# Kernel optimization log

Measured on AMD Instinct MI355X. Metric: run time of the kernel, lower is better.

The kernel has to match this reference:

```python
import jax, jax.numpy as jnp
import numpy as np
from jax.scipy.special import logsumexp

B, T, D, H, K = 64, 800, 80, 128, 39  # batch, frames, feat dim, LSTM hidden/dir, num phones


def setup_inputs() -> dict:
    key = jax.random.key(0)
    ks = jax.random.split(key, 16)
    s = 0.1
    inp = {
        "features": jax.random.normal(ks[0], (B, T, D), jnp.float32),
        "lengths": jax.random.randint(ks[1], (B,), T // 2, T + 1, dtype=jnp.int32),
        "labels": jax.random.randint(ks[2], (B, T), 0, K, dtype=jnp.int32),
        # BiLSTM params (PyTorch layout: W_ih (4H,D), W_hh (4H,H); gate order i,f,g,o)
        "Wih_f": jax.random.normal(ks[3], (4 * H, D), jnp.float32) * s,
        "Whh_f": jax.random.normal(ks[4], (4 * H, H), jnp.float32) * s,
        "bih_f": jax.random.normal(ks[5], (4 * H,), jnp.float32) * s,
        "bhh_f": jax.random.normal(ks[6], (4 * H,), jnp.float32) * s,
        "Wih_b": jax.random.normal(ks[7], (4 * H, D), jnp.float32) * s,
        "Whh_b": jax.random.normal(ks[8], (4 * H, H), jnp.float32) * s,
        "bih_b": jax.random.normal(ks[9], (4 * H,), jnp.float32) * s,
        "bhh_b": jax.random.normal(ks[10], (4 * H,), jnp.float32) * s,
        # emission projection Linear(2H -> K)
        "Wp": jax.random.normal(ks[11], (K, 2 * H), jnp.float32) * s,
        "bp": jax.random.normal(ks[12], (K,), jnp.float32) * s,
        # CRF params (pytorch-crf init: U(-0.1, 0.1))
        "start_t": jax.random.uniform(ks[13], (K,), jnp.float32, -0.1, 0.1),
        "end_t": jax.random.uniform(ks[14], (K,), jnp.float32, -0.1, 0.1),
        "trans": jax.random.uniform(ks[15], (K, K), jnp.float32, -0.1, 0.1),
    }
    return inp


def _lstm(x, Wih, Whh, bih, bhh, reverse):
    """Single-direction LSTM over padded batch. x: (B,T,D) -> (B,T,H)."""
    nB, nT, _ = x.shape
    nH = Whh.shape[1]
    xW = jnp.swapaxes(x @ Wih.T + (bih + bhh), 0, 1)  # (T,B,4H)

    def step(carry, g):
        h, c = carry
        g = g + h @ Whh.T
        i, f, gg, o = jnp.split(g, 4, axis=-1)
        c = jax.nn.sigmoid(f) * c + jax.nn.sigmoid(i) * jnp.tanh(gg)
        h = jax.nn.sigmoid(o) * jnp.tanh(c)
        return (h, c), h

    init = (jnp.zeros((nB, nH), x.dtype), jnp.zeros((nB, nH), x.dtype))
    _, hs = jax.lax.scan(step, init, xW, reverse=reverse)
    return jnp.swapaxes(hs, 0, 1)  # (B,T,H)


def _crf_nll(emissions, labels, lengths, start_t, end_t, trans):
    """pytorch-crf: -mean log-likelihood. emissions (B,T,K), labels (B,T)."""
    nB, nT, nK = emissions.shape
    mask = (jnp.arange(nT)[None, :] < lengths[:, None])  # (B,T)
    mf = mask.astype(emissions.dtype)
    bidx = jnp.arange(nB)

    # --- numerator: score of gold path ---
    num = start_t[labels[:, 0]] + emissions[bidx, 0, labels[:, 0]]
    tr = trans[labels[:, :-1], labels[:, 1:]]  # (B,T-1)
    em = jnp.take_along_axis(emissions[:, 1:], labels[:, 1:, None], axis=2)[..., 0]
    num = num + ((tr + em) * mf[:, 1:]).sum(axis=1)
    last_tags = jnp.take_along_axis(labels, (lengths - 1)[:, None], axis=1)[:, 0]
    num = num + end_t[last_tags]

    # --- denominator: forward algorithm ---
    alpha0 = start_t[None, :] + emissions[:, 0]  # (B,K)
    em_rest = jnp.swapaxes(emissions[:, 1:], 0, 1)  # (T-1,B,K)
    m_rest = jnp.swapaxes(mask[:, 1:], 0, 1)  # (T-1,B)

    def step(alpha, inputs):
        em_t, m_t = inputs
        nxt = logsumexp(alpha[:, :, None] + trans[None] + em_t[:, None, :], axis=1)
        return jnp.where(m_t[:, None], nxt, alpha), None

    alpha, _ = jax.lax.scan(step, alpha0, (em_rest, m_rest))
    denom = logsumexp(alpha + end_t[None, :], axis=1)

    return -(num - denom).mean()


def reference(features, lengths, labels, Wih_f, Whh_f, bih_f, bhh_f,
              Wih_b, Whh_b, bih_b, bhh_b, Wp, bp, start_t, end_t, trans):
    h_f = _lstm(features, Wih_f, Whh_f, bih_f, bhh_f, reverse=False)
    h_b = _lstm(features, Wih_b, Whh_b, bih_b, bhh_b, reverse=True)
    hidden = jnp.concatenate([h_f, h_b], axis=-1)  # (B,T,2H)
    emissions = hidden @ Wp.T + bp  # (B,T,K)
    return _crf_nll(emissions, labels, lengths, start_t, end_t, trans)
```

## Files before the change

### kernel.cpp

```cpp
#include <hip/hip_runtime.h>
#include <cstddef>
#include <cstdint>

#define B_ 64
#define T_ 800
#define D_ 80
#define H_ 128
#define K_ 39
#define BT_ (B_ * T_)

#define NL2E_  (-1.44269504f)
#define N2L2E_ (-2.88539008f)

typedef _Float16 h2_t  __attribute__((ext_vector_type(2)));
typedef _Float16 f16x8 __attribute__((ext_vector_type(8)));
typedef float    f32x4 __attribute__((ext_vector_type(4)));
typedef uint32_t u32x4 __attribute__((ext_vector_type(4)));

__device__ __forceinline__ float fdot2_(h2_t a, h2_t b, float c) {
#if __has_builtin(__builtin_amdgcn_fdot2)
  return __builtin_amdgcn_fdot2(a, b, c, false);
#else
  return c + (float)a.x * (float)b.x + (float)a.y * (float)b.y;
#endif
}

__device__ __forceinline__ h2_t asH2u_(uint32_t u) { return __builtin_bit_cast(h2_t, u); }

__device__ __forceinline__ float ex2_(float x) {
#if __has_builtin(__builtin_amdgcn_exp2f)
  return __builtin_amdgcn_exp2f(x);
#else
  return __builtin_exp2f(x);
#endif
}
__device__ __forceinline__ float rcpf_(float x) {
#if __has_builtin(__builtin_amdgcn_rcpf)
  return __builtin_amdgcn_rcpf(x);
#else
  return 1.0f / x;
#endif
}
__device__ __forceinline__ float tanhf_(float x) { return 2.0f / (1.0f + __expf(-2.0f * x)) - 1.0f; }

__device__ __forceinline__ float laneb_(float v, int lane) {
  return __builtin_bit_cast(float, __builtin_amdgcn_readlane(__builtin_bit_cast(int, v), lane));
}
__device__ __forceinline__ uint32_t lanebu_(uint32_t v, int lane) {
  return (uint32_t)__builtin_amdgcn_readlane((int)v, lane);
}

__device__ __forceinline__ float dppswap1_(float v) {
  return __builtin_bit_cast(float,
    __builtin_amdgcn_mov_dpp(__builtin_bit_cast(int, v), 0xB1, 0xF, 0xF, true));
}

__device__ __forceinline__ void barrier_lds_() {
  asm volatile("s_waitcnt lgkmcnt(0)" ::: "memory");
  __builtin_amdgcn_s_barrier();
}

__device__ __forceinline__ void rows_of_(int tid, int& unit, int& role, int& r0, int& r1) {
  const int w = tid >> 6, L = tid & 63;
  unit = w * 32 + (L >> 1);
  role = L & 1;
  r0 = role * H_ + unit;
  r1 = 2 * H_ + role * H_ + unit;
}

template<int USE_XW>
__global__ __launch_bounds__(256, 1)
void lstm_kernel(const float* __restrict__ x,
                 const float* __restrict__ Wih_f, const float* __restrict__ Whh_f,
                 const float* __restrict__ bih_f, const float* __restrict__ bhh_f,
                 const float* __restrict__ Wih_b, const float* __restrict__ Whh_b,
                 const float* __restrict__ bih_b, const float* __restrict__ bhh_b,
                 _Float16* __restrict__ xw,
                 _Float16* __restrict__ hcat)
{
  const int bb  = blockIdx.x & 63;
  const int dir = blockIdx.x >> 6;
  const float* Whh = dir ? Whh_b : Whh_f;
  const float* Wih = dir ? Wih_b : Wih_f;
  const float* bih = dir ? bih_b : bih_f;
  const float* bhh = dir ? bhh_b : bhh_f;

  const int tid  = threadIdx.x;
  const int lane = tid & 63;

  __shared__ alignas(16) _Float16 hsf[2][H_];
  __shared__ uint32_t xs2[2][64];
  __shared__ alignas(16) _Float16 xs[128 * 96];

  if (USE_XW) {
    const int w    = tid >> 6;
    const int lm   = lane & 15;
    const int quad = lane >> 4;
    const int selw = w >> 1;
    const int rolw = w & 1;

    f16x8 Bf[8][3];
    #pragma unroll
    for (int nt = 0; nt < 8; ++nt) {
      const int r = w * 128 + nt * 16 + lm;
      const float fac = (r >= 256 && r < 384) ? N2L2E_ : NL2E_;
      #pragma unroll
      for (int kt = 0; kt < 3; ++kt) {
        const int kb = kt * 32 + quad * 8;
        #pragma unroll
        for (int j = 0; j < 8; ++j) {
          const int k = kb + j;
          Bf[nt][kt][j] = (k < D_) ? (_Float16)(fac * Wih[(size_t)r * D_ + k]) : (_Float16)0.0f;
        }
      }
    }

    for (int i = tid; i < 128 * 96; i += 256) xs[i] = (_Float16)0.0f;

    for (int cc = 0; cc < 7; ++cc) {
      const int base = cc * 128;
      const int nrow = (T_ - base < 128) ? (T_ - base) : 128;
      __syncthreads();
      {
        const float4* src = (const float4*)(x + ((size_t)bb * T_ + base) * D_);
        for (int i = tid; i < nrow * 20; i += 256) {
          float4 v = src[i];
          const int row = i / 20, col = (i % 20) * 4;
          h2_t p0, p1;
          p0.x = (_Float16)v.x; p0.y = (_Float16)v.y;
          p1.x = (_Float16)v.z; p1.y = (_Float16)v.w;
          uint2 pk;
          pk.x = __builtin_bit_cast(uint32_t, p0);
          pk.y = __builtin_bit_cast(uint32_t, p1);
          *(uint2*)&xs[row * 96 + col] = pk;
        }
      }
      __syncthreads();

      #pragma unroll
      for (int mt = 0; mt < 8; ++mt) {
        if (base + mt * 16 >= T_) break;
        f16x8 Af[3];
        #pragma unroll
        for (int kt = 0; kt < 3; ++kt)
          Af[kt] = *(const f16x8*)&xs[(mt * 16 + lm) * 96 + kt * 32 + quad * 8];

        f32x4 acc[8];
        #pragma unroll
        for (int nt = 0; nt < 8; ++nt) acc[nt] = (f32x4){0.f, 0.f, 0.f, 0.f};
        #pragma unroll
        for (int kt = 0; kt < 3; ++kt)
          #pragma unroll
          for (int nt = 0; nt < 8; ++nt)
            acc[nt] = __builtin_amdgcn_mfma_f32_16x16x32_f16(Af[kt], Bf[nt][kt], acc[nt], 0, 0, 0);

        #pragma unroll
        for (int nt = 0; nt < 8; ++nt) {
          const int unit = nt * 16 + lm;
          const int ptid = (unit >> 5) * 64 + (unit & 31) * 2 + rolw;
          #pragma unroll
          for (int rg = 0; rg < 4; ++rg) {
            const int t = base + mt * 16 + quad * 4 + rg;
            if (t < T_)
              xw[((size_t)dir * BT_ + (size_t)bb * T_ + t) * 512 + ptid * 2 + selw]
                = (_Float16)acc[nt][rg];
          }
        }
      }
    }
    __syncthreads();
  }

  const int Q = lane & 3; (void)Q;
  int unit, role, r0, r1; rows_of_(tid, unit, role, r0, r1);
  const float s0 = NL2E_;
  const float s1 = role ? NL2E_ : N2L2E_;
  const float qk2 = role ? 0.0f : -1.0f;

  h2_t w0[64], w1[64];
  #pragma unroll
  for (int j = 0; j < 64; ++j) {
    float2 a = *(const float2*)(Whh + (size_t)r0 * H_ + 2 * j);
    float2 d = *(const float2*)(Whh + (size_t)r1 * H_ + 2 * j);
    w0[j].x = (_Float16)(s0 * a.x); w0[j].y = (_Float16)(s0 * a.y);
    w1[j].x = (_Float16)(s1 * d.x); w1[j].y = (_Float16)(s1 * d.y);
  }
  h2_t wx0[40], wx1[40];
  if (!USE_XW) {
    #pragma unroll
    for (int i = 0; i < 40; ++i) {
      float2 a = *(const float2*)(Wih + (size_t)r0 * D_ + 2 * i);
      float2 d = *(const float2*)(Wih + (size_t)r1 * D_ + 2 * i);
      wx0[i].x = (_Float16)(s0 * a.x); wx0[i].y = (_Float16)(s0 * a.y);
      wx1[i].x = (_Float16)(s1 * d.x); wx1[i].y = (_Float16)(s1 * d.y);
    }
  }
  const float bias0 = s0 * (bih[r0] + bhh[r0]);
  const float bias1 = s1 * (bih[r1] + bhh[r1]);

  if (tid < H_) hsf[0][tid] = (_Float16)0.0f;
  if (!USE_XW && tid < 64) { xs2[0][tid] = 0u; xs2[1][tid] = 0u; }
  float c = 0.0f;

  const uint32_t* xwdu = (const uint32_t*)xw + ((size_t)dir * BT_ + (size_t)bb * T_) * 256;
  const float*    xb   = x + (size_t)bb * T_ * D_;
  _Float16*       hb   = hcat + (size_t)bb * T_ * (2 * H_) + dir * H_;

  _Float16* hbp = hb + (size_t)(dir ? (T_ - 1) : 0) * (2 * H_);
  const ptrdiff_t hstep = dir ? -(2 * H_) : (2 * H_);
  int xoff = (dir ? (T_ - 3) : 2) * 256 + tid;
  const int xstep = dir ? -256 : 256;

  uint32_t xwA = 0u, xwB = 0u;
  h2_t xpend; xpend.x = (_Float16)0.f; xpend.y = (_Float16)0.f;
  {
    const int tq0 = dir ? (T_ - 1) : 0;
    const int tq1 = dir ? (T_ - 2) : 1;
    if (USE_XW) {
      xwA = xwdu[(size_t)tq0 * 256 + tid];
      xwB = xwdu[(size_t)tq1 * 256 + tid];
    } else if (tid < 40) {
      float2 v0 = *(const float2*)(xb + (size_t)tq0 * D_ + 2 * tid);
      h2_t p; p.x = (_Float16)v0.x; p.y = (_Float16)v0.y;
      xs2[0][tid] = __builtin_bit_cast(uint32_t, p);
      float2 v1 = *(const float2*)(xb + (size_t)tq1 * D_ + 2 * tid);
      xpend.x = (_Float16)v1.x; xpend.y = (_Float16)v1.y;
    }
  }
  __syncthreads();

  auto step = [&](int tt, int par, uint32_t& xwreg) {
    float a0, a1, a2, a3, b0, b1, b2, b3;
    if (USE_XW) {
      const h2_t xv = asH2u_(xwreg);
      a0 = bias0 + (float)xv.x;
      b0 = bias1 + (float)xv.y;
      a1 = a2 = a3 = 0.f; b1 = b2 = b3 = 0.f;
      xwreg = xwdu[xoff];
    } else {
      a0 = bias0; b0 = bias1;
      a1 = a2 = a3 = 0.f; b1 = b2 = b3 = 0.f;
      if (tid < 40) {
        xs2[par ^ 1][tid] = __builtin_bit_cast(uint32_t, xpend);
        const int ttc = (tt + 2 < T_) ? (tt + 2) : (T_ - 1);
        const int tq2 = dir ? (T_ - 1 - ttc) : ttc;
        float2 v = *(const float2*)(xb + (size_t)tq2 * D_ + 2 * tid);
        xpend.x = (_Float16)v.x; xpend.y = (_Float16)v.y;
      }
      uint32_t xreg = xs2[par][lane];
      #pragma unroll
      for (int j = 0; j < 40; j += 4) {
        h2_t q0 = asH2u_(lanebu_(xreg, j));
        h2_t q1 = asH2u_(lanebu_(xreg, j + 1));
        h2_t q2 = asH2u_(lanebu_(xreg, j + 2));
        h2_t q3 = asH2u_(lanebu_(xreg, j + 3));
        a0 = fdot2_(wx0[j],     q0, a0); b0 = fdot2_(wx1[j],     q0, b0);
        a1 = fdot2_(wx0[j + 1], q1, a1); b1 = fdot2_(wx1[j + 1], q1, b1);
        a2 = fdot2_(wx0[j + 2], q2, a2); b2 = fdot2_(wx1[j + 2], q2, b2);
        a3 = fdot2_(wx0[j + 3], q3, a3); b3 = fdot2_(wx1[j + 3], q3, b3);
      }
    }

    const u32x4* hq = (const u32x4*)hsf[par];
    #pragma unroll
    for (int g = 0; g < 16; ++g) {
      const u32x4 hv = hq[g];
      a0 = fdot2_(w0[4 * g + 0], asH2u_(hv[0]), a0);
      b0 = fdot2_(w1[4 * g + 0], asH2u_(hv[0]), b0);
      a1 = fdot2_(w0[4 * g + 1], asH2u_(hv[1]), a1);
      b1 = fdot2_(w1[4 * g + 1], asH2u_(hv[1]), b1);
      a2 = fdot2_(w0[4 * g + 2], asH2u_(hv[2]), a2);
      b2 = fdot2_(w1[4 * g + 2], asH2u_(hv[2]), b2);
      a3 = fdot2_(w0[4 * g + 3], asH2u_(hv[3]), a3);
      b3 = fdot2_(w1[4 * g + 3], asH2u_(hv[3]), b3);
    }
    const float ga = (a0 + a1) + (a2 + a3);
    const float gb = (b0 + b1) + (b2 + b3);

    const float ea = ex2_(ga);
    const float sg = rcpf_(1.0f + ea);
    const float gbc = fminf(fmaxf(gb, -34.6f), 34.6f);
    const float eb = ex2_(gbc);
    const float qv = fmaf(qk2, eb, 1.0f) * rcpf_(1.0f + eb);
    const float ex = dppswap1_(sg * qv);
    c = fmaf(sg, c, ex);
    const float hn = qv * tanhf_(c);
    if (role) {
      hsf[par ^ 1][unit] = (_Float16)hn;
      hbp[unit] = (_Float16)hn;
    }
    hbp += hstep;
    if (tt + 3 < T_) xoff += xstep;
    barrier_lds_();
  };

  for (int tb = 0; tb < T_; tb += 2) {
    step(tb,     0, xwA);
    step(tb + 1, 1, xwB);
  }
}

__global__ __launch_bounds__(256, 1)
void emis_kernel(const _Float16* __restrict__ hcat,
                 const float* __restrict__ Wp, const float* __restrict__ bp,
                 float* __restrict__ em)
{
  const int tid  = threadIdx.x;
  const int w    = tid >> 6;
  const int lane = tid & 63;
  const int lm   = lane & 15;
  const int quad = lane >> 4;

  f16x8 Bf[3][8];
  float bias[3];
  #pragma unroll
  for (int nt = 0; nt < 3; ++nt) {
    const int n = nt * 16 + lm;
    const bool valid = n < K_;
    bias[nt] = valid ? bp[n] : 0.0f;
    #pragma unroll
    for (int kt = 0; kt < 8; ++kt) {
      const int kb = kt * 32 + quad * 8;
      #pragma unroll
      for (int j = 0; j < 8; ++j)
        Bf[nt][kt][j] = valid ? (_Float16)Wp[(size_t)n * 256 + kb + j] : (_Float16)0.0f;
    }
  }

  #pragma unroll
  for (int q = 0; q < 4; ++q) {
    const int mt  = blockIdx.x * 16 + w * 4 + q;
    const int bt0 = mt * 16;

    f16x8 Af[8];
    const _Float16* ab = hcat + ((size_t)bt0 + lm) * 256;
    #pragma unroll
    for (int kt = 0; kt < 8; ++kt)
      Af[kt] = *(const f16x8*)(ab + kt * 32 + quad * 8);

    f32x4 acc[3];
    #pragma unroll
    for (int nt = 0; nt < 3; ++nt) acc[nt] = (f32x4){0.f, 0.f, 0.f, 0.f};
    #pragma unroll
    for (int kt = 0; kt < 8; ++kt)
      #pragma unroll
      for (int nt = 0; nt < 3; ++nt)
        acc[nt] = __builtin_amdgcn_mfma_f32_16x16x32_f16(Af[kt], Bf[nt][kt], acc[nt], 0, 0, 0);

    #pragma unroll
    for (int nt = 0; nt < 3; ++nt) {
      const int n = nt * 16 + lm;
      if (n < K_) {
        #pragma unroll
        for (int rg = 0; rg < 4; ++rg) {
          const int row = bt0 + quad * 4 + rg;
          em[(size_t)row * K_ + n] = acc[nt][rg] + bias[nt];
        }
      }
    }
  }
}

__global__ __launch_bounds__(256)
void crf_dn_kernel(const float* __restrict__ em,
                   const int* __restrict__ labels, const int* __restrict__ lengths,
                   const float* __restrict__ start_t, const float* __restrict__ end_t,
                   const float* __restrict__ trans,
                   float* __restrict__ dn)
{
  const int b    = blockIdx.x;
  const int tid  = threadIdx.x;
  const int wv   = tid >> 6;
  const int lane = tid & 63;
  const int len  = lengths[b];
  const float* emb = em + (size_t)b * T_ * K_;

  __shared__ float s_num[3];
  __shared__ float s_den;

  if (wv == 0) {
    float et[K_];
    #pragma unroll
    for (int j = 0; j < K_; ++j)
      et[j] = (lane < K_) ? __expf(trans[j * K_ + lane]) : 0.0f;

    float a0 = (lane < K_) ? (start_t[lane] + emb[lane]) : -1e30f;
    float m = a0;
    #pragma unroll
    for (int off = 32; off > 0; off >>= 1) m = fmaxf(m, __shfl_xor(m, off));
    float v = __expf(a0 - m);
    float off_acc = m;

    auto ldc = [&](int t) -> float {
      const int tc = (t < len) ? t : (len - 1);
      return (lane < K_) ? emb[(size_t)tc * K_ + lane] : 0.0f;
    };

    float eA = ldc(1), eB = ldc(2), eC = ldc(3), eD = ldc(4);
    float eE = ldc(5), eF = ldc(6), eG = ldc(7), eH = ldc(8);

    auto stepden = [&](float& ereg, int tt) {
      const float emc = ereg;
      ereg = ldc(tt + 8);
      if (tt < len) {
        const float pv = v;
        float s0 = 0.f, s1 = 0.f, s2 = 0.f, s3 = 0.f;
        #pragma unroll
        for (int j = 0; j < 36; j += 4) {
          s0 = fmaf(laneb_(pv, j),     et[j],     s0);
          s1 = fmaf(laneb_(pv, j + 1), et[j + 1], s1);
          s2 = fmaf(laneb_(pv, j + 2), et[j + 2], s2);
          s3 = fmaf(laneb_(pv, j + 3), et[j + 3], s3);
        }
        s0 = fmaf(laneb_(pv, 36), et[36], s0);
        s1 = fmaf(laneb_(pv, 37), et[37], s1);
        s2 = fmaf(laneb_(pv, 38), et[38], s2);
        v = ((s0 + s1) + (s2 + s3)) * __expf(emc);
        if ((tt & 3) == 0) {
          const float sc = laneb_(v, 0);
          v *= 1.0f / sc;
          off_acc += __logf(sc);
        }
      }
    };

    for (int t = 1; t < len; t += 8) {
      stepden(eA, t);     stepden(eB, t + 1);
      stepden(eC, t + 2); stepden(eD, t + 3);
      stepden(eE, t + 4); stepden(eF, t + 5);
      stepden(eG, t + 6); stepden(eH, t + 7);
    }

    float w = (lane < K_) ? v * __expf(end_t[lane]) : 0.0f;
    #pragma unroll
    for (int off = 32; off > 0; off >>= 1) w += __shfl_xor(w, off);
    if (lane == 0) s_den = off_acc + __logf(w);
  } else {
    const int idx = tid - 64;
    float acc = 0.0f;
    for (int t = 1 + idx; t < len; t += 192) {
      const int lp = labels[b * T_ + t - 1];
      const int lc = labels[b * T_ + t];
      acc += trans[lp * K_ + lc] + emb[(size_t)t * K_ + lc];
    }
    if (tid == 64) {
      const int l0 = labels[b * T_];
      const int ll = labels[b * T_ + len - 1];
      acc += start_t[l0] + emb[l0] + end_t[ll];
    }
    #pragma unroll
    for (int off = 32; off > 0; off >>= 1) acc += __shfl_xor(acc, off);
    if (lane == 0) s_num[wv - 1] = acc;
  }
  __syncthreads();
  if (tid == 0) dn[b] = s_den - (s_num[0] + s_num[1] + s_num[2]);
}

__global__ void finalize_kernel(const float* __restrict__ dn, float* __restrict__ out)
{
  const int tid = threadIdx.x;
  float v = dn[tid];
  #pragma unroll
  for (int off = 32; off > 0; off >>= 1) v += __shfl_down(v, off);
  if (tid == 0) out[0] = v * (1.0f / 64.0f);
}

extern "C" void kernel_launch(void* const* d_in, const int* in_sizes, int n_in,
                              void* d_out, int out_size, void* d_ws, size_t ws_size,
                              hipStream_t stream)
{
  (void)in_sizes; (void)n_in; (void)out_size;
  const float* features = (const float*)d_in[0];
  const int*   lengths  = (const int*)d_in[1];
  const int*   labels   = (const int*)d_in[2];
  const float* Wih_f = (const float*)d_in[3];
  const float* Whh_f = (const float*)d_in[4];
  const float* bih_f = (const float*)d_in[5];
  const float* bhh_f = (const float*)d_in[6];
  const float* Wih_b = (const float*)d_in[7];
  const float* Whh_b = (const float*)d_in[8];
  const float* bih_b = (const float*)d_in[9];
  const float* bhh_b = (const float*)d_in[10];
  const float* Wp      = (const float*)d_in[11];
  const float* bp      = (const float*)d_in[12];
  const float* start_t = (const float*)d_in[13];
  const float* end_t   = (const float*)d_in[14];
  const float* trans   = (const float*)d_in[15];
  float* out = (float*)d_out;

  char* wsc = (char*)d_ws;
  _Float16* hcatH = (_Float16*)wsc;
  float*    em    = (float*)(wsc + 26214400);
  float*    dn    = (float*)(wsc + 26214400 + 7987200);
  _Float16* xwH   = (_Float16*)(wsc + 34202112);
  const bool big  = ws_size >= (size_t)34202112 + 104857600;

  if (big) {
    hipLaunchKernelGGL((lstm_kernel<1>), dim3(2 * B_), dim3(256), 0, stream,
                       features, Wih_f, Whh_f, bih_f, bhh_f,
                       Wih_b, Whh_b, bih_b, bhh_b, xwH, hcatH);
  } else {
    hipLaunchKernelGGL((lstm_kernel<0>), dim3(2 * B_), dim3(256), 0, stream,
                       features, Wih_f, Whh_f, bih_f, bhh_f,
                       Wih_b, Whh_b, bih_b, bhh_b, xwH, hcatH);
  }
  hipLaunchKernelGGL(emis_kernel, dim3(BT_ / 256), dim3(256), 0, stream,
                     hcatH, Wp, bp, em);
  hipLaunchKernelGGL(crf_dn_kernel, dim3(B_), dim3(256), 0, stream,
                     em, labels, lengths, start_t, end_t, trans, dn);
  hipLaunchKernelGGL(finalize_kernel, dim3(1), dim3(64), 0, stream,
                     dn, out);
}
```

Baseline: 769.0 us.

## Interleave input-projection GEMM chunks into LSTM recurrence via LDS buffer

Replaces the upfront full-sequence input projection, which was written to a large global workspace and streamed back per step, with 32-timestep MFMA GEMM chunks computed inside the recurrence loop into an LDS ring buffer. The W_ih fragments are staged in LDS instead of registers. This removes the global round trip for xw and the serialized prologue, and relaxes the workspace requirement. In exchange it adds a barrier and GEMM work every 32 steps on the critical recurrent path, uses much more LDS, and the x-add now happens after the dot products.

```diff
diff --git a/kernel.cpp b/kernel.cpp
--- a/kernel.cpp
+++ b/kernel.cpp
@@ -75,7 +75,6 @@
                  const float* __restrict__ bih_f, const float* __restrict__ bhh_f,
                  const float* __restrict__ Wih_b, const float* __restrict__ Whh_b,
                  const float* __restrict__ bih_b, const float* __restrict__ bhh_b,
-                 _Float16* __restrict__ xw,
                  _Float16* __restrict__ hcat)
 {
   const int bb  = blockIdx.x & 63;
@@ -87,91 +86,33 @@
 
   const int tid  = threadIdx.x;
   const int lane = tid & 63;
+  const int wv   = tid >> 6;
+  const int lm   = lane & 15;
+  const int quad = lane >> 4;
 
   __shared__ alignas(16) _Float16 hsf[2][H_];
   __shared__ uint32_t xs2[2][64];
-  __shared__ alignas(16) _Float16 xs[128 * 96];
+  __shared__ alignas(16) _Float16 Wfrag[96 * 512];
+  __shared__ alignas(16) _Float16 xwl[32][512];
 
   if (USE_XW) {
-    const int w    = tid >> 6;
-    const int lm   = lane & 15;
-    const int quad = lane >> 4;
-    const int selw = w >> 1;
-    const int rolw = w & 1;
-
-    f16x8 Bf[8][3];
     #pragma unroll
     for (int nt = 0; nt < 8; ++nt) {
-      const int r = w * 128 + nt * 16 + lm;
+      const int r = wv * 128 + nt * 16 + lm;
       const float fac = (r >= 256 && r < 384) ? N2L2E_ : NL2E_;
       #pragma unroll
       for (int kt = 0; kt < 3; ++kt) {
         const int kb = kt * 32 + quad * 8;
+        f16x8 f;
         #pragma unroll
-        for (int j = 0; j < 8; ++j) {
-          const int k = kb + j;
-          Bf[nt][kt][j] = (k < D_) ? (_Float16)(fac * Wih[(size_t)r * D_ + k]) : (_Float16)0.0f;
-        }
-      }
-    }
-
-    for (int i = tid; i < 128 * 96; i += 256) xs[i] = (_Float16)0.0f;
-
-    for (int cc = 0; cc < 7; ++cc) {
-      const int base = cc * 128;
-      const int nrow = (T_ - base < 128) ? (T_ - base) : 128;
-      __syncthreads();
-      {
-        const float4* src = (const float4*)(x + ((size_t)bb * T_ + base) * D_);
-        for (int i = tid; i < nrow * 20; i += 256) {
-          float4 v = src[i];
-          const int row = i / 20, col = (i % 20) * 4;
-          h2_t p0, p1;
-          p0.x = (_Float16)v.x; p0.y = (_Float16)v.y;
-          p1.x = (_Float16)v.z; p1.y = (_Float16)v.w;
-          uint2 pk;
-          pk.x = __builtin_bit_cast(uint32_t, p0);
-          pk.y = __builtin_bit_cast(uint32_t, p1);
-          *(uint2*)&xs[row * 96 + col] = pk;
-        }
-      }
-      __syncthreads();
-
-      #pragma unroll
-      for (int mt = 0; mt < 8; ++mt) {
-        if (base + mt * 16 >= T_) break;
-        f16x8 Af[3];
-        #pragma unroll
-        for (int kt = 0; kt < 3; ++kt)
-          Af[kt] = *(const f16x8*)&xs[(mt * 16 + lm) * 96 + kt * 32 + quad * 8];
-
-        f32x4 acc[8];
-        #pragma unroll
-        for (int nt = 0; nt < 8; ++nt) acc[nt] = (f32x4){0.f, 0.f, 0.f, 0.f};
-        #pragma unroll
-        for (int kt = 0; kt < 3; ++kt)
-          #pragma unroll
-          for (int nt = 0; nt < 8; ++nt)
-            acc[nt] = __builtin_amdgcn_mfma_f32_16x16x32_f16(Af[kt], Bf[nt][kt], acc[nt], 0, 0, 0);
-
-        #pragma unroll
-        for (int nt = 0; nt < 8; ++nt) {
-          const int unit = nt * 16 + lm;
-          const int ptid = (unit >> 5) * 64 + (unit & 31) * 2 + rolw;
-          #pragma unroll
-          for (int rg = 0; rg < 4; ++rg) {
-            const int t = base + mt * 16 + quad * 4 + rg;
-            if (t < T_)
-              xw[((size_t)dir * BT_ + (size_t)bb * T_ + t) * 512 + ptid * 2 + selw]
-                = (_Float16)acc[nt][rg];
-          }
-        }
-      }
-    }
-    __syncthreads();
-  }
-
-  const int Q = lane & 3; (void)Q;
+        for (int j = 0; j < 8; ++j)
+          f[j] = (kb < D_) ? (_Float16)(fac * Wih[(size_t)r * D_ + kb + j])
+                           : (_Float16)0.0f;
+        *(f16x8*)&Wfrag[(((wv * 8 + nt) * 3 + kt) << 9) + lane * 8] = f;
+      }
+    }
+  }
+
   int unit, role, r0, r1; rows_of_(tid, unit, role, r0, r1);
   const float s0 = NL2E_;
   const float s1 = role ? NL2E_ : N2L2E_;
@@ -202,41 +143,72 @@
   if (!USE_XW && tid < 64) { xs2[0][tid] = 0u; xs2[1][tid] = 0u; }
   float c = 0.0f;
 
-  const uint32_t* xwdu = (const uint32_t*)xw + ((size_t)dir * BT_ + (size_t)bb * T_) * 256;
-  const float*    xb   = x + (size_t)bb * T_ * D_;
-  _Float16*       hb   = hcat + (size_t)bb * T_ * (2 * H_) + dir * H_;
-
-  _Float16* hbp = hb + (size_t)(dir ? (T_ - 1) : 0) * (2 * H_);
+  const float* xb = x + (size_t)bb * T_ * D_;
+  _Float16*    hb = hcat + (size_t)bb * T_ * (2 * H_) + dir * H_;
+  _Float16*    hbp = hb + (size_t)(dir ? (T_ - 1) : 0) * (2 * H_);
   const ptrdiff_t hstep = dir ? -(2 * H_) : (2 * H_);
-  int xoff = (dir ? (T_ - 3) : 2) * 256 + tid;
-  const int xstep = dir ? -256 : 256;
-
-  uint32_t xwA = 0u, xwB = 0u;
+
   h2_t xpend; xpend.x = (_Float16)0.f; xpend.y = (_Float16)0.f;
-  {
+  if (!USE_XW && tid < 40) {
     const int tq0 = dir ? (T_ - 1) : 0;
     const int tq1 = dir ? (T_ - 2) : 1;
-    if (USE_XW) {
-      xwA = xwdu[(size_t)tq0 * 256 + tid];
-      xwB = xwdu[(size_t)tq1 * 256 + tid];
-    } else if (tid < 40) {
-      float2 v0 = *(const float2*)(xb + (size_t)tq0 * D_ + 2 * tid);
-      h2_t p; p.x = (_Float16)v0.x; p.y = (_Float16)v0.y;
-      xs2[0][tid] = __builtin_bit_cast(uint32_t, p);
-      float2 v1 = *(const float2*)(xb + (size_t)tq1 * D_ + 2 * tid);
-      xpend.x = (_Float16)v1.x; xpend.y = (_Float16)v1.y;
-    }
+    float2 v0 = *(const float2*)(xb + (size_t)tq0 * D_ + 2 * tid);
+    h2_t p; p.x = (_Float16)v0.x; p.y = (_Float16)v0.y;
+    xs2[0][tid] = __builtin_bit_cast(uint32_t, p);
+    float2 v1 = *(const float2*)(xb + (size_t)tq1 * D_ + 2 * tid);
+    xpend.x = (_Float16)v1.x; xpend.y = (_Float16)v1.y;
   }
   __syncthreads();
 
-  auto step = [&](int tt, int par, uint32_t& xwreg) {
+  auto gemm_chunk = [&](int tb) {
+    const int base_t = dir ? (T_ - 32 - tb) : tb;
+    #pragma unroll
+    for (int mt = 0; mt < 2; ++mt) {
+      const float* xr = xb + (size_t)(base_t + mt * 16 + lm) * D_;
+      f16x8 Af[3];
+      #pragma unroll
+      for (int kt = 0; kt < 3; ++kt) {
+        const int kb = kt * 32 + quad * 8;
+        if (kb < D_) {
+          float4 v0 = *(const float4*)(xr + kb);
+          float4 v1 = *(const float4*)(xr + kb + 4);
+          Af[kt][0] = (_Float16)v0.x; Af[kt][1] = (_Float16)v0.y;
+          Af[kt][2] = (_Float16)v0.z; Af[kt][3] = (_Float16)v0.w;
+          Af[kt][4] = (_Float16)v1.x; Af[kt][5] = (_Float16)v1.y;
+          Af[kt][6] = (_Float16)v1.z; Af[kt][7] = (_Float16)v1.w;
+        } else {
+          #pragma unroll
+          for (int j = 0; j < 8; ++j) Af[kt][j] = (_Float16)0.0f;
+        }
+      }
+      #pragma unroll
+      for (int nt = 0; nt < 8; ++nt) {
+        f32x4 acc = (f32x4){0.f, 0.f, 0.f, 0.f};
+        #pragma unroll
+        for (int kt = 0; kt < 3; ++kt) {
+          const f16x8 Bf = *(const f16x8*)&Wfrag[(((wv * 8 + nt) * 3 + kt) << 9) + lane * 8];
+          acc = __builtin_amdgcn_mfma_f32_16x16x32_f16(Af[kt], Bf, acc, 0, 0, 0);
+        }
+        const int un   = nt * 16 + lm;
+        const int pidx = ((un >> 5) * 64 + (un & 31) * 2 + (wv & 1)) * 2 + (wv >> 1);
+        #pragma unroll
+        for (int rg = 0; rg < 4; ++rg) {
+          const int lr   = mt * 16 + quad * 4 + rg;
+          const int slot = dir ? (31 - lr) : lr;
+          xwl[slot][pidx] = (_Float16)acc[rg];
+        }
+      }
+    }
+    barrier_lds_();
+  };
+
+  auto step = [&](int tt, int par) {
+    uint32_t xvu = 0u;
     float a0, a1, a2, a3, b0, b1, b2, b3;
     if (USE_XW) {
-      const h2_t xv = asH2u_(xwreg);
-      a0 = bias0 + (float)xv.x;
-      b0 = bias1 + (float)xv.y;
+      xvu = ((const uint32_t*)xwl)[((tt & 31) << 8) + tid];
+      a0 = bias0; b0 = bias1;
       a1 = a2 = a3 = 0.f; b1 = b2 = b3 = 0.f;
-      xwreg = xwdu[xoff];
     } else {
       a0 = bias0; b0 = bias1;
       a1 = a2 = a3 = 0.f; b1 = b2 = b3 = 0.f;
@@ -274,8 +246,13 @@
       a3 = fdot2_(w0[4 * g + 3], asH2u_(hv[3]), a3);
       b3 = fdot2_(w1[4 * g + 3], asH2u_(hv[3]), b3);
     }
-    const float ga = (a0 + a1) + (a2 + a3);
-    const float gb = (b0 + b1) + (b2 + b3);
+    float ga = (a0 + a1) + (a2 + a3);
+    float gb = (b0 + b1) + (b2 + b3);
+    if (USE_XW) {
+      const h2_t xv = asH2u_(xvu);
+      ga += (float)xv.x;
+      gb += (float)xv.y;
+    }
 
     const float ea = ex2_(ga);
     const float sg = rcpf_(1.0f + ea);
@@ -290,13 +267,13 @@
       hbp[unit] = (_Float16)hn;
     }
     hbp += hstep;
-    if (tt + 3 < T_) xoff += xstep;
     barrier_lds_();
   };
 
   for (int tb = 0; tb < T_; tb += 2) {
-    step(tb,     0, xwA);
-    step(tb + 1, 1, xwB);
+    if (USE_XW && (tb & 31) == 0) gemm_chunk(tb);
+    step(tb,     0);
+    step(tb + 1, 1);
   }
 }
 
@@ -492,17 +469,16 @@
   _Float16* hcatH = (_Float16*)wsc;
   float*    em    = (float*)(wsc + 26214400);
   float*    dn    = (float*)(wsc + 26214400 + 7987200);
-  _Float16* xwH   = (_Float16*)(wsc + 34202112);
-  const bool big  = ws_size >= (size_t)34202112 + 104857600;
+  const bool big  = ws_size >= (size_t)34202112;
 
   if (big) {
     hipLaunchKernelGGL((lstm_kernel<1>), dim3(2 * B_), dim3(256), 0, stream,
                        features, Wih_f, Whh_f, bih_f, bhh_f,
-                       Wih_b, Whh_b, bih_b, bhh_b, xwH, hcatH);
+                       Wih_b, Whh_b, bih_b, bhh_b, hcatH);
   } else {
     hipLaunchKernelGGL((lstm_kernel<0>), dim3(2 * B_), dim3(256), 0, stream,
                        features, Wih_f, Whh_f, bih_f, bhh_f,
-                       Wih_b, Whh_b, bih_b, bhh_b, xwH, hcatH);
+                       Wih_b, Whh_b, bih_b, bhh_b, hcatH);
   }
   hipLaunchKernelGGL(emis_kernel, dim3(BT_ / 256), dim3(256), 0, stream,
                      hcatH, Wp, bp, em);
```

After: 875.1 us. 1.14x slower.
